# Kernel tuning notes

Hardware: AMD Instinct MI355X
Metric: run time of the kernel (lower is better)

Reference implementation:

```python
import jax, jax.numpy as jnp
import numpy as np

B, C_IN, C_OUT, H, W, K, NK = 16, 256, 256, 64, 64, 3, 2
EPS = 1e-8


def setup_inputs() -> dict:
    key = jax.random.key(0)
    k1, k2, k3, k4 = jax.random.split(key, 4)
    x = jax.random.normal(k1, (B, C_IN, H, W), dtype=jnp.float32)
    mod = jax.random.normal(k2, (B, C_IN), dtype=jnp.float32)
    kernel_mod = jax.random.normal(k3, (B, NK), dtype=jnp.float32)
    # kernel bank: [num_conv_kernels, dim_out, dim_in, k, k] (kaiming-ish scale)
    weights = jax.random.normal(k4, (NK, C_OUT, C_IN, K, K), dtype=jnp.float32) / np.sqrt(C_IN * K * K)
    gamma = jnp.ones((C_OUT,), dtype=jnp.float32)
    return {"x": x, "mod": mod, "kernel_mod": kernel_mod, "weights": weights, "gamma": gamma}


def _block(x, mod, kernel_mod, weights, gamma):
    # adaptive kernel selection: softmax-mix the kernel bank per sample
    attn = jax.nn.softmax(kernel_mod, axis=-1)                       # [b, n]
    w = jnp.einsum('bn,noikl->boikl', attn, weights)                 # [b, o, i, k, k]
    # style modulation over input channels
    w = w * (mod[:, None, :, None, None] + 1.0)
    # demodulation
    denom = jnp.clip(jnp.sum(w * w, axis=(2, 3, 4), keepdims=True), EPS)
    w = w * jax.lax.rsqrt(denom)
    # per-sample conv (groups=b trick in torch) -> vmap over batch
    def conv_one(fmap, wb):
        return jax.lax.conv_general_dilated(
            fmap[None], wb, window_strides=(1, 1), padding='SAME',
            dimension_numbers=('NCHW', 'OIHW', 'NCHW'))[0]
    y = jax.vmap(conv_one)(x, w)                                     # [b, o, h, w]
    # RMSNorm over channel dim: F.normalize(x, dim=1) * gamma * sqrt(dim)
    norm = jnp.sqrt(jnp.sum(y * y, axis=1, keepdims=True))
    y = y / jnp.maximum(norm, 1e-12)
    y = y * gamma[None, :, None, None] * (gamma.shape[0] ** 0.5)
    # SiLU
    return y * jax.nn.sigmoid(y)


def reference(x, mod, kernel_mod, weights, gamma):
    return _block(x, mod, kernel_mod, weights, gamma)
```

## Files before the change

kernel.cpp:

```cpp
#include <hip/hip_runtime.h>
#include <math.h>


typedef __attribute__((ext_vector_type(8))) short short8;
typedef __attribute__((ext_vector_type(4))) float f32x4;

#define GLL16(src, dst)                                                       \
  __builtin_amdgcn_global_load_lds(                                           \
      (const __attribute__((address_space(1))) unsigned int*)(src),           \
      (__attribute__((address_space(3))) unsigned int*)(dst), 16, 0, 0)

static __device__ __forceinline__ unsigned short f2bf(float v) {
  union { float f; unsigned u; } u;
  u.f = v;
  unsigned r = u.u + 0x7FFF + ((u.u >> 16) & 1);
  return (unsigned short)(r >> 16);
}

__global__ __launch_bounds__(256) void scale_kernel(
    const float* __restrict__ mod, const float* __restrict__ kmod,
    const float* __restrict__ weights, float* __restrict__ scale) {
  int bo = blockIdx.x;
  int b = bo >> 8, o = bo & 255;

  float k0 = kmod[b * 2 + 0], k1 = kmod[b * 2 + 1];
  float mx = fmaxf(k0, k1);
  float e0 = expf(k0 - mx), e1 = expf(k1 - mx);
  float ai = 1.0f / (e0 + e1);
  float a0 = e0 * ai, a1 = e1 * ai;

  int t = threadIdx.x;
  const float* w0 = weights + (size_t)o * 2304;
  const float* w1 = w0 + 589824;

  float s = 0.0f;
#pragma unroll
  for (int r = 0; r < 9; r++) {
    int idx = t + r * 256;
    int i = idx / 9;
    float wv = a0 * w0[idx] + a1 * w1[idx];
    wv *= (mod[b * 256 + i] + 1.0f);
    s += wv * wv;
  }
#pragma unroll
  for (int off = 32; off > 0; off >>= 1) s += __shfl_down(s, off);

  __shared__ float red[4];
  if ((t & 63) == 0) red[t >> 6] = s;
  __syncthreads();
  if (t == 0) {
    float tot = red[0] + red[1] + red[2] + red[3];
    scale[bo] = rsqrtf(fmaxf(tot, 1e-8f));
  }
}

__global__ __launch_bounds__(256) void wprep(
    const float* __restrict__ mod, const float* __restrict__ kmod,
    const float* __restrict__ weights, const float* __restrict__ scale,
    unsigned short* __restrict__ wq) {
  __shared__ __align__(16) unsigned short buf[20480];
  int blk = blockIdx.x;
  int b = blk >> 5, ot = (blk >> 4) & 1, c = blk & 15;
  int t = threadIdx.x;

  float k0 = kmod[b * 2 + 0], k1 = kmod[b * 2 + 1];
  float mx = fmaxf(k0, k1);
  float e0 = expf(k0 - mx), e1 = expf(k1 - mx);
  float ai = 1.0f / (e0 + e1);
  float a0 = e0 * ai, a1 = e1 * ai;

#pragma unroll
  for (int k = 0; k < 8; ++k) {
    int e = t + k * 256;
    int half = e >> 10;
    buf[(half * 10 + 9) * 1024 + (e & 1023)] = 0;
  }

  int ol = t >> 1, eh = t & 1;
  int o = ot * 128 + ol;
  float sc = scale[b * 256 + o];
#pragma unroll
  for (int io = 0; io < 2; ++io) {
#pragma unroll
    for (int eo = 0; eo < 4; ++eo) {
      int e = eh * 4 + eo;
      int i = c * 16 + io * 8 + e;
      float f = (mod[b * 256 + i] + 1.0f) * sc;
      const float* w0 = &weights[((size_t)o * 256 + i) * 9];
      const float* w1 = w0 + 589824;
#pragma unroll
      for (int j = 0; j < 9; ++j) {
        float v = (a0 * w0[j] + a1 * w1[j]) * f;
        buf[(io * 10 + j) * 1024 + ol * 8 + e] = f2bf(v);
      }
    }
  }
  __syncthreads();
  size_t base = (size_t)blk * 20480;
#pragma unroll
  for (int k = 0; k < 10; ++k) {
    int idx = t + k * 256;
    *(short8*)(wq + base + (size_t)idx * 8) = *(const short8*)&buf[idx * 8];
  }
}

__global__ __launch_bounds__(256) void xprep(
    const float* __restrict__ x, unsigned short* __restrict__ xq) {
  int blk = blockIdx.x;
  int rowp = blk % 66;
  int bc = blk / 66;
  int b = bc >> 4, c = bc & 15;
  int t = threadIdx.x;
  size_t obase = (size_t)blk * 1056;

  if (rowp == 0 || rowp == 65) {
    for (int idx = t; idx < 1056; idx += 256) xq[obase + idx] = 0;
    return;
  }
  __shared__ __align__(16) unsigned short xs2[1056];
  int row = rowp - 1;
  for (int idx = t; idx < 1056; idx += 256) xs2[idx] = 0;
  __syncthreads();
#pragma unroll
  for (int k = 0; k < 4; ++k) {
    int idx = t + k * 256;
    int il = idx >> 6, col = idx & 63;
    float v = x[(((size_t)b * 256 + c * 16 + il) * 64 + row) * 64 + col];
    xs2[(col + 1) * 16 + il] = f2bf(v);
  }
  __syncthreads();
  if (t < 132) *(short8*)(xq + obase + (size_t)t * 8) = *(const short8*)&xs2[t * 8];
}

__global__ __launch_bounds__(512, 2) void conv_mfma(
    const unsigned short* __restrict__ xq, const unsigned short* __restrict__ wq,
    float* __restrict__ out) {
  __shared__ __align__(16) unsigned short wsm[2][20480];
  __shared__ __align__(16) unsigned short xsm[2][15840];

  int bid = blockIdx.x;
  int b = bid >> 4, ot = (bid >> 3) & 1, rt = bid & 7;
  int grp = b * 2 + ot;
  int r0 = rt * 8;

  int t = threadIdx.x;
  int w = t >> 6, lane = t & 63;
  int g = (t >> 4) & 3, lm = t & 15;

  int baddr_[5], aaddr_[5];
#pragma unroll
  for (int s = 0; s < 5; ++s) {
    int p = 4 * s + g;
    int io = (p >= 10) ? 1 : 0;
    int j = p - 10 * io;
    int jd3, jm3;
    if (j == 9) { jd3 = 0; jm3 = 0; }
    else { jd3 = (j >= 3) + (j >= 6); jm3 = j - 3 * jd3; }
    baddr_[s] = ((w + jd3) * 66 + lm + jm3) * 48 + io * 16;
    aaddr_[s] = p * 2048 + lm * 16;
  }

  int xo0, xo1, xo2;
  {
    int i0 = t, i1 = t + 512, i2 = t + 1024;
    int rl, rem;
    rl = i0 / 132; rem = i0 - rl * 132; xo0 = (rl * 66 + (rem >> 1)) * 24 + (rem & 1) * 8;
    rl = i1 / 132; rem = i1 - rl * 132; xo1 = (rl * 66 + (rem >> 1)) * 24 + (rem & 1) * 8;
    rl = i2 / 132; rem = i2 - rl * 132; xo2 = (rl * 66 + (rem >> 1)) * 24 + (rem & 1) * 8;
  }

  f32x4 acc[8][4];
#pragma unroll
  for (int mf = 0; mf < 8; ++mf)
#pragma unroll
    for (int nf = 0; nf < 4; ++nf) acc[mf][nf] = (f32x4){0.f, 0.f, 0.f, 0.f};

  short8 xr0, xr1, xr2;

#define XLOAD(cn)                                                              \
  {                                                                            \
    const unsigned short* xs_ = xq + (size_t)(((b * 16 + (cn)) * 66 + r0)) * 1056; \
    xr0 = *(const short8*)(xs_ + (size_t)t * 8);                               \
    xr1 = *(const short8*)(xs_ + (size_t)(t + 512) * 8);                       \
    if (t < 296) xr2 = *(const short8*)(xs_ + (size_t)(t + 1024) * 8);         \
  }

#define WSTAGE(cn, nb)                                                         \
  {                                                                            \
    const unsigned short* ws_ =                                                \
        wq + ((size_t)grp * 16 + (cn)) * 20480 + (w * 5) * 512 + lane * 8;     \
    unsigned short* wd_ = &wsm[nb][(w * 5) * 512];                             \
    _Pragma("unroll")                                                          \
    for (int it = 0; it < 5; ++it) GLL16(ws_ + it * 512, wd_ + it * 512);      \
  }

#define XWRITE(nb)                                                             \
  {                                                                            \
    *(short8*)&xsm[nb][xo0] = xr0;                                             \
    *(short8*)&xsm[nb][xo1] = xr1;                                             \
    if (t < 296) *(short8*)&xsm[nb][xo2] = xr2;                                \
  }

  XLOAD(0);
  WSTAGE(0, 0);
  XWRITE(0);
  __syncthreads();

  for (int c = 0; c < 16; ++c) {
    int cur = c & 1;
    if (c < 15) {
      XLOAD(c + 1);
      WSTAGE(c + 1, cur ^ 1);
    }
    {
      const char* wsb = (const char*)wsm[cur];
      const char* xsb = (const char*)xsm[cur];
#pragma unroll
      for (int s = 0; s < 5; ++s) {
        short8 A[8];
#pragma unroll
        for (int mf = 0; mf < 8; ++mf)
          A[mf] = *(const short8*)(wsb + aaddr_[s] + mf * 256);
#pragma unroll
        for (int nf = 0; nf < 4; ++nf) {
          short8 Bf = *(const short8*)(xsb + baddr_[s] + nf * 768);
#pragma unroll
          for (int mf = 0; mf < 8; ++mf)
            acc[mf][nf] =
                __builtin_amdgcn_mfma_f32_16x16x32_bf16(A[mf], Bf, acc[mf][nf], 0, 0, 0);
        }
      }
    }
    if (c < 15) XWRITE(cur ^ 1);
    __syncthreads();
  }

  int row = r0 + w;
#pragma unroll
  for (int mf = 0; mf < 8; ++mf)
#pragma unroll
    for (int nf = 0; nf < 4; ++nf)
#pragma unroll
      for (int q = 0; q < 4; ++q) {
        int o = ot * 128 + mf * 16 + g * 4 + q;
        int col = nf * 16 + lm;
        out[(((size_t)b * 256 + o) * 64 + row) * 64 + col] = acc[mf][nf][q];
      }
#undef XLOAD
#undef WSTAGE
#undef XWRITE
}

__global__ __launch_bounds__(256) void norm_kernel(
    float* __restrict__ y, const float* __restrict__ gamma) {
  int blk = blockIdx.x;
  int b = blk >> 6, h = blk & 63;
  int t = threadIdx.x;
  int p = t & 63, og = t >> 6;

  size_t base = (((size_t)b * 256) * 64 + h) * 64 + p;
  float yv[64];
  float s = 0.0f;
#pragma unroll
  for (int k = 0; k < 64; k++) {
    yv[k] = y[base + (size_t)(og * 64 + k) * 4096];
    s = fmaf(yv[k], yv[k], s);
  }

  __shared__ float red[4][64];
  __shared__ float invs[64];
  red[og][p] = s;
  __syncthreads();
  if (og == 0) {
    float tot = red[0][p] + red[1][p] + red[2][p] + red[3][p];
    float nrm = sqrtf(tot);
    invs[p] = 16.0f / fmaxf(nrm, 1e-12f);
  }
  __syncthreads();
  float iv = invs[p];
#pragma unroll
  for (int k = 0; k < 64; k++) {
    int o = og * 64 + k;
    float v = yv[k] * iv * gamma[o];
    float sg = 1.0f / (1.0f + expf(-v));
    y[base + (size_t)o * 4096] = v * sg;
  }
}

extern "C" void kernel_launch(void* const* d_in, const int* in_sizes, int n_in,
                              void* d_out, int out_size, void* d_ws, size_t ws_size,
                              hipStream_t stream) {
  const float* x = (const float*)d_in[0];
  const float* mod = (const float*)d_in[1];
  const float* kmod = (const float*)d_in[2];
  const float* weights = (const float*)d_in[3];
  const float* gamma = (const float*)d_in[4];
  float* out = (float*)d_out;

  unsigned short* wq = (unsigned short*)d_ws;
  float* scale = (float*)((char*)d_ws + 20971520);
  unsigned short* xq = (unsigned short*)((char*)d_ws + 20987904);

  scale_kernel<<<16 * 256, 256, 0, stream>>>(mod, kmod, weights, scale);
  wprep<<<512, 256, 0, stream>>>(mod, kmod, weights, scale, wq);
  xprep<<<16 * 16 * 66, 256, 0, stream>>>(x, xq);
  conv_mfma<<<256, 512, 0, stream>>>(xq, wq, out);
  norm_kernel<<<16 * 64, 256, 0, stream>>>(out, gamma);
}
```

Baseline: 143.0 us.

## Shrink conv tiles to 64 outputs x 4 rows and remap blocks per XCD

The conv kernel moves from 256 blocks of 512 threads (128 output channels x 8 rows) to 1024 blocks of 256 threads (64 channels x 4 rows). The weight prep layout is repacked to match. Block indices are remapped so that each XCD handles two batches, keeping that data within one L2. The intent is to fill all CUs on the MI355X, since 256 blocks underfill the 256 CUs when two blocks fit per CU. The cost is less reuse per tile: x halo rows get reloaded for each channel tile and the loads-to-MFMA ratio rises.

```diff
diff --git a/kernel.cpp b/kernel.cpp
--- a/kernel.cpp
+++ b/kernel.cpp
@@ -58,9 +58,9 @@
     const float* __restrict__ mod, const float* __restrict__ kmod,
     const float* __restrict__ weights, const float* __restrict__ scale,
     unsigned short* __restrict__ wq) {
-  __shared__ __align__(16) unsigned short buf[20480];
+  __shared__ __align__(16) unsigned short buf[10240];
   int blk = blockIdx.x;
-  int b = blk >> 5, ot = (blk >> 4) & 1, c = blk & 15;
+  int b = blk >> 6, ot = (blk >> 4) & 3, c = blk & 15;
   int t = threadIdx.x;
 
   float k0 = kmod[b * 2 + 0], k1 = kmod[b * 2 + 1];
@@ -70,20 +70,20 @@
   float a0 = e0 * ai, a1 = e1 * ai;
 
 #pragma unroll
-  for (int k = 0; k < 8; ++k) {
+  for (int k = 0; k < 4; ++k) {
     int e = t + k * 256;
-    int half = e >> 10;
-    buf[(half * 10 + 9) * 1024 + (e & 1023)] = 0;
-  }
-
-  int ol = t >> 1, eh = t & 1;
-  int o = ot * 128 + ol;
+    int half = e >> 9;
+    buf[(half * 10 + 9) * 512 + (e & 511)] = 0;
+  }
+
+  int ol = t >> 2, q = t & 3;
+  int o = ot * 64 + ol;
   float sc = scale[b * 256 + o];
 #pragma unroll
   for (int io = 0; io < 2; ++io) {
 #pragma unroll
-    for (int eo = 0; eo < 4; ++eo) {
-      int e = eh * 4 + eo;
+    for (int e2 = 0; e2 < 2; ++e2) {
+      int e = q * 2 + e2;
       int i = c * 16 + io * 8 + e;
       float f = (mod[b * 256 + i] + 1.0f) * sc;
       const float* w0 = &weights[((size_t)o * 256 + i) * 9];
@@ -91,14 +91,14 @@
 #pragma unroll
       for (int j = 0; j < 9; ++j) {
         float v = (a0 * w0[j] + a1 * w1[j]) * f;
-        buf[(io * 10 + j) * 1024 + ol * 8 + e] = f2bf(v);
+        buf[(io * 10 + j) * 512 + ol * 8 + e] = f2bf(v);
       }
     }
   }
   __syncthreads();
-  size_t base = (size_t)blk * 20480;
-#pragma unroll
-  for (int k = 0; k < 10; ++k) {
+  size_t base = (size_t)blk * 10240;
+#pragma unroll
+  for (int k = 0; k < 5; ++k) {
     int idx = t + k * 256;
     *(short8*)(wq + base + (size_t)idx * 8) = *(const short8*)&buf[idx * 8];
   }
@@ -132,16 +132,20 @@
   if (t < 132) *(short8*)(xq + obase + (size_t)t * 8) = *(const short8*)&xs2[t * 8];
 }
 
-__global__ __launch_bounds__(512, 2) void conv_mfma(
+__global__ __launch_bounds__(256, 2) void conv_mfma(
     const unsigned short* __restrict__ xq, const unsigned short* __restrict__ wq,
     float* __restrict__ out) {
-  __shared__ __align__(16) unsigned short wsm[2][20480];
-  __shared__ __align__(16) unsigned short xsm[2][15840];
+  __shared__ __align__(16) unsigned short wsm[2][10240];
+  __shared__ __align__(16) unsigned short xsm[2][9504];
 
   int bid = blockIdx.x;
-  int b = bid >> 4, ot = (bid >> 3) & 1, rt = bid & 7;
-  int grp = b * 2 + ot;
-  int r0 = rt * 8;
+  int xcd = bid & 7;
+  int kk = bid >> 3;
+  int b = xcd * 2 + (kk >> 6);
+  int rem = kk & 63;
+  int ot = rem >> 4;
+  int rt = rem & 15;
+  int r0 = rt * 4;
 
   int t = threadIdx.x;
   int w = t >> 6, lane = t & 63;
@@ -157,39 +161,41 @@
     if (j == 9) { jd3 = 0; jm3 = 0; }
     else { jd3 = (j >= 3) + (j >= 6); jm3 = j - 3 * jd3; }
     baddr_[s] = ((w + jd3) * 66 + lm + jm3) * 48 + io * 16;
-    aaddr_[s] = p * 2048 + lm * 16;
-  }
-
-  int xo0, xo1, xo2;
+    aaddr_[s] = p * 1024 + lm * 16;
+  }
+
+  int xo0, xo1, xo2, xo3;
   {
-    int i0 = t, i1 = t + 512, i2 = t + 1024;
-    int rl, rem;
-    rl = i0 / 132; rem = i0 - rl * 132; xo0 = (rl * 66 + (rem >> 1)) * 24 + (rem & 1) * 8;
-    rl = i1 / 132; rem = i1 - rl * 132; xo1 = (rl * 66 + (rem >> 1)) * 24 + (rem & 1) * 8;
-    rl = i2 / 132; rem = i2 - rl * 132; xo2 = (rl * 66 + (rem >> 1)) * 24 + (rem & 1) * 8;
-  }
-
-  f32x4 acc[8][4];
-#pragma unroll
-  for (int mf = 0; mf < 8; ++mf)
+    int idx, rl, rm;
+    idx = t;        rl = idx / 132; rm = idx - rl * 132; xo0 = (rl * 66 + (rm >> 1)) * 24 + (rm & 1) * 8;
+    idx = t + 256;  rl = idx / 132; rm = idx - rl * 132; xo1 = (rl * 66 + (rm >> 1)) * 24 + (rm & 1) * 8;
+    idx = t + 512;  rl = idx / 132; rm = idx - rl * 132; xo2 = (rl * 66 + (rm >> 1)) * 24 + (rm & 1) * 8;
+    idx = t + 768;  rl = idx / 132; rm = idx - rl * 132; xo3 = (rl * 66 + (rm >> 1)) * 24 + (rm & 1) * 8;
+  }
+
+  f32x4 acc[4][4];
+#pragma unroll
+  for (int mf = 0; mf < 4; ++mf)
 #pragma unroll
     for (int nf = 0; nf < 4; ++nf) acc[mf][nf] = (f32x4){0.f, 0.f, 0.f, 0.f};
 
-  short8 xr0, xr1, xr2;
+  short8 xr0, xr1, xr2, xr3;
 
 #define XLOAD(cn)                                                              \
   {                                                                            \
-    const unsigned short* xs_ = xq + (size_t)(((b * 16 + (cn)) * 66 + r0)) * 1056; \
+    const unsigned short* xs_ =                                                \
+        xq + (size_t)((b * 16 + (cn)) * 66 + r0) * 1056;                       \
     xr0 = *(const short8*)(xs_ + (size_t)t * 8);                               \
-    xr1 = *(const short8*)(xs_ + (size_t)(t + 512) * 8);                       \
-    if (t < 296) xr2 = *(const short8*)(xs_ + (size_t)(t + 1024) * 8);         \
+    xr1 = *(const short8*)(xs_ + (size_t)(t + 256) * 8);                       \
+    xr2 = *(const short8*)(xs_ + (size_t)(t + 512) * 8);                       \
+    if (t < 24) xr3 = *(const short8*)(xs_ + (size_t)(t + 768) * 8);           \
   }
 
 #define WSTAGE(cn, nb)                                                         \
   {                                                                            \
     const unsigned short* ws_ =                                                \
-        wq + ((size_t)grp * 16 + (cn)) * 20480 + (w * 5) * 512 + lane * 8;     \
-    unsigned short* wd_ = &wsm[nb][(w * 5) * 512];                             \
+        wq + ((size_t)(b * 4 + ot) * 16 + (cn)) * 10240 + w * 2560 + lane * 8; \
+    unsigned short* wd_ = &wsm[nb][w * 2560];                                  \
     _Pragma("unroll")                                                          \
     for (int it = 0; it < 5; ++it) GLL16(ws_ + it * 512, wd_ + it * 512);      \
   }
@@ -198,7 +204,8 @@
   {                                                                            \
     *(short8*)&xsm[nb][xo0] = xr0;                                             \
     *(short8*)&xsm[nb][xo1] = xr1;                                             \
-    if (t < 296) *(short8*)&xsm[nb][xo2] = xr2;                                \
+    *(short8*)&xsm[nb][xo2] = xr2;                                             \
+    if (t < 24) *(short8*)&xsm[nb][xo3] = xr3;                                 \
   }
 
   XLOAD(0);
@@ -217,15 +224,15 @@
       const char* xsb = (const char*)xsm[cur];
 #pragma unroll
       for (int s = 0; s < 5; ++s) {
-        short8 A[8];
-#pragma unroll
-        for (int mf = 0; mf < 8; ++mf)
+        short8 A[4];
+#pragma unroll
+        for (int mf = 0; mf < 4; ++mf)
           A[mf] = *(const short8*)(wsb + aaddr_[s] + mf * 256);
 #pragma unroll
         for (int nf = 0; nf < 4; ++nf) {
           short8 Bf = *(const short8*)(xsb + baddr_[s] + nf * 768);
 #pragma unroll
-          for (int mf = 0; mf < 8; ++mf)
+          for (int mf = 0; mf < 4; ++mf)
             acc[mf][nf] =
                 __builtin_amdgcn_mfma_f32_16x16x32_bf16(A[mf], Bf, acc[mf][nf], 0, 0, 0);
         }
@@ -237,12 +244,12 @@
 
   int row = r0 + w;
 #pragma unroll
-  for (int mf = 0; mf < 8; ++mf)
+  for (int mf = 0; mf < 4; ++mf)
 #pragma unroll
     for (int nf = 0; nf < 4; ++nf)
 #pragma unroll
       for (int q = 0; q < 4; ++q) {
-        int o = ot * 128 + mf * 16 + g * 4 + q;
+        int o = ot * 64 + mf * 16 + g * 4 + q;
         int col = nf * 16 + lm;
         out[(((size_t)b * 256 + o) * 64 + row) * 64 + col] = acc[mf][nf][q];
       }
@@ -302,8 +309,8 @@
   unsigned short* xq = (unsigned short*)((char*)d_ws + 20987904);
 
   scale_kernel<<<16 * 256, 256, 0, stream>>>(mod, kmod, weights, scale);
-  wprep<<<512, 256, 0, stream>>>(mod, kmod, weights, scale, wq);
+  wprep<<<1024, 256, 0, stream>>>(mod, kmod, weights, scale, wq);
   xprep<<<16 * 16 * 66, 256, 0, stream>>>(x, xq);
-  conv_mfma<<<256, 512, 0, stream>>>(xq, wq, out);
+  conv_mfma<<<1024, 256, 0, stream>>>(xq, wq, out);
   norm_kernel<<<16 * 64, 256, 0, stream>>>(out, gamma);
 }
```

New measurement: 139.4 us. 2.5% less time.

## Stage activations via direct global-to-LDS loads with pre-swizzled layout and XCD-aware block mapping

Applied to the files above, without the earlier changes.

The x-prep kernel now writes its packed bf16 rows with a per-16-byte XOR flip, so the conv kernel can copy activation tiles straight into LDS with global_load_lds instead of going through registers and a padded 48-byte-stride layout. The conv reads apply the matching swizzle to avoid bank conflicts, and LDS use per buffer shrinks. Async loads for the next channel chunk are spread across the first MFMA sub-steps, with s_setprio around the MFMA bursts and a vmcnt wait plus barrier at the end of each chunk. Block IDs are remapped so that blocks sharing a batch sample land on the same XCD, which should improve L2 reuse. The risk is that the swizzle written by the producer and the one read by the consumer must match exactly.

```diff
diff --git a/kernel.cpp b/kernel.cpp
--- a/kernel.cpp
+++ b/kernel.cpp
@@ -129,18 +129,26 @@
     xs2[(col + 1) * 16 + il] = f2bf(v);
   }
   __syncthreads();
-  if (t < 132) *(short8*)(xq + obase + (size_t)t * 8) = *(const short8*)&xs2[t * 8];
+  if (t < 132) {
+    int G = blk * 132 + t;
+    int flip = ((G >> 3) & 1) ^ (bc & 1);
+    *(short8*)(xq + obase + (size_t)(t ^ flip) * 8) = *(const short8*)&xs2[t * 8];
+  }
 }
 
 __global__ __launch_bounds__(512, 2) void conv_mfma(
     const unsigned short* __restrict__ xq, const unsigned short* __restrict__ wq,
     float* __restrict__ out) {
   __shared__ __align__(16) unsigned short wsm[2][20480];
-  __shared__ __align__(16) unsigned short xsm[2][15840];
+  __shared__ __align__(16) unsigned short xsm[2][10560];
 
   int bid = blockIdx.x;
-  int b = bid >> 4, ot = (bid >> 3) & 1, rt = bid & 7;
-  int grp = b * 2 + ot;
+  int xcd = bid & 7;
+  int kk = bid >> 3;
+  int b = xcd * 2 + (kk >> 4);
+  int rem = kk & 15;
+  int ot = rem >> 3;
+  int rt = rem & 7;
   int r0 = rt * 8;
 
   int t = threadIdx.x;
@@ -156,83 +164,68 @@
     int jd3, jm3;
     if (j == 9) { jd3 = 0; jm3 = 0; }
     else { jd3 = (j >= 3) + (j >= 6); jm3 = j - 3 * jd3; }
-    baddr_[s] = ((w + jd3) * 66 + lm + jm3) * 48 + io * 16;
+    int ba = ((w + jd3) * 66 + lm + jm3) * 32 + io * 16;
+    ba ^= ((ba >> 7) & 1) << 4;
+    baddr_[s] = ba;
     aaddr_[s] = p * 2048 + lm * 16;
   }
 
-  int xo0, xo1, xo2;
-  {
-    int i0 = t, i1 = t + 512, i2 = t + 1024;
-    int rl, rem;
-    rl = i0 / 132; rem = i0 - rl * 132; xo0 = (rl * 66 + (rem >> 1)) * 24 + (rem & 1) * 8;
-    rl = i1 / 132; rem = i1 - rl * 132; xo1 = (rl * 66 + (rem >> 1)) * 24 + (rem & 1) * 8;
-    rl = i2 / 132; rem = i2 - rl * 132; xo2 = (rl * 66 + (rem >> 1)) * 24 + (rem & 1) * 8;
-  }
-
   f32x4 acc[8][4];
 #pragma unroll
   for (int mf = 0; mf < 8; ++mf)
 #pragma unroll
     for (int nf = 0; nf < 4; ++nf) acc[mf][nf] = (f32x4){0.f, 0.f, 0.f, 0.f};
 
-  short8 xr0, xr1, xr2;
-
-#define XLOAD(cn)                                                              \
+#define WGLL(cn, nb, r)                                                        \
   {                                                                            \
-    const unsigned short* xs_ = xq + (size_t)(((b * 16 + (cn)) * 66 + r0)) * 1056; \
-    xr0 = *(const short8*)(xs_ + (size_t)t * 8);                               \
-    xr1 = *(const short8*)(xs_ + (size_t)(t + 512) * 8);                       \
-    if (t < 296) xr2 = *(const short8*)(xs_ + (size_t)(t + 1024) * 8);         \
-  }
-
-#define WSTAGE(cn, nb)                                                         \
+    const unsigned short* s_ = wq + ((size_t)(b * 32 + ot * 16 + (cn))) * 20480 \
+                               + ((r) * 512 + w * 64 + lane) * 8;              \
+    GLL16(s_, &wsm[nb][(r) * 4096 + w * 512]);                                 \
+  }
+#define XGLL(cn, nb, r)                                                        \
   {                                                                            \
-    const unsigned short* ws_ =                                                \
-        wq + ((size_t)grp * 16 + (cn)) * 20480 + (w * 5) * 512 + lane * 8;     \
-    unsigned short* wd_ = &wsm[nb][(w * 5) * 512];                             \
-    _Pragma("unroll")                                                          \
-    for (int it = 0; it < 5; ++it) GLL16(ws_ + it * 512, wd_ + it * 512);      \
-  }
-
-#define XWRITE(nb)                                                             \
-  {                                                                            \
-    *(short8*)&xsm[nb][xo0] = xr0;                                             \
-    *(short8*)&xsm[nb][xo1] = xr1;                                             \
-    if (t < 296) *(short8*)&xsm[nb][xo2] = xr2;                                \
-  }
-
-  XLOAD(0);
-  WSTAGE(0, 0);
-  XWRITE(0);
-  __syncthreads();
+    const unsigned short* s_ = xq + ((size_t)((b * 16 + (cn)) * 66 + r0)) * 1056 \
+                               + ((r) * 512 + w * 64 + lane) * 8;              \
+    GLL16(s_, &xsm[nb][(r) * 4096 + w * 512]);                                 \
+  }
+
+  WGLL(0, 0, 0); WGLL(0, 0, 1); WGLL(0, 0, 2); WGLL(0, 0, 3); WGLL(0, 0, 4);
+  XGLL(0, 0, 0); XGLL(0, 0, 1);
+  if (t < 296) XGLL(0, 0, 2);
+  asm volatile("s_waitcnt vmcnt(0)" ::: "memory");
+  __builtin_amdgcn_s_barrier();
+  __builtin_amdgcn_sched_barrier(0);
 
   for (int c = 0; c < 16; ++c) {
     int cur = c & 1;
-    if (c < 15) {
-      XLOAD(c + 1);
-      WSTAGE(c + 1, cur ^ 1);
+    const char* wsb = (const char*)wsm[cur];
+    const char* xsb = (const char*)xsm[cur];
+#pragma unroll
+    for (int s = 0; s < 5; ++s) {
+      if (c < 15) {
+        int nb = cur ^ 1;
+        if (s == 0) { WGLL(c + 1, nb, 0); WGLL(c + 1, nb, 1); XGLL(c + 1, nb, 0); }
+        if (s == 1) { WGLL(c + 1, nb, 2); WGLL(c + 1, nb, 3); XGLL(c + 1, nb, 1); }
+        if (s == 2) { WGLL(c + 1, nb, 4); if (t < 296) XGLL(c + 1, nb, 2); }
+      }
+      short8 A[8];
+#pragma unroll
+      for (int mf = 0; mf < 8; ++mf)
+        A[mf] = *(const short8*)(wsb + aaddr_[s] + mf * 256);
+      __builtin_amdgcn_s_setprio(1);
+#pragma unroll
+      for (int nf = 0; nf < 4; ++nf) {
+        short8 Bf = *(const short8*)(xsb + baddr_[s] + nf * 512);
+#pragma unroll
+        for (int mf = 0; mf < 8; ++mf)
+          acc[mf][nf] =
+              __builtin_amdgcn_mfma_f32_16x16x32_bf16(A[mf], Bf, acc[mf][nf], 0, 0, 0);
+      }
+      __builtin_amdgcn_s_setprio(0);
     }
-    {
-      const char* wsb = (const char*)wsm[cur];
-      const char* xsb = (const char*)xsm[cur];
-#pragma unroll
-      for (int s = 0; s < 5; ++s) {
-        short8 A[8];
-#pragma unroll
-        for (int mf = 0; mf < 8; ++mf)
-          A[mf] = *(const short8*)(wsb + aaddr_[s] + mf * 256);
-#pragma unroll
-        for (int nf = 0; nf < 4; ++nf) {
-          short8 Bf = *(const short8*)(xsb + baddr_[s] + nf * 768);
-#pragma unroll
-          for (int mf = 0; mf < 8; ++mf)
-            acc[mf][nf] =
-                __builtin_amdgcn_mfma_f32_16x16x32_bf16(A[mf], Bf, acc[mf][nf], 0, 0, 0);
-        }
-      }
-    }
-    if (c < 15) XWRITE(cur ^ 1);
-    __syncthreads();
+    asm volatile("s_waitcnt vmcnt(0)" ::: "memory");
+    __builtin_amdgcn_s_barrier();
+    __builtin_amdgcn_sched_barrier(0);
   }
 
   int row = r0 + w;
@@ -246,9 +239,8 @@
         int col = nf * 16 + lm;
         out[(((size_t)b * 256 + o) * 64 + row) * 64 + col] = acc[mf][nf][q];
       }
-#undef XLOAD
-#undef WSTAGE
-#undef XWRITE
+#undef WGLL
+#undef XGLL
 }
 
 __global__ __launch_bounds__(256) void norm_kernel(
```

New measurement: 142.3 us. About the same (-0.5%).
